# Kernel tuning notes

Measured on AMD Instinct MI355X. Metric: run time of the kernel, lower is better.

Reference implementation:

```python
import jax, jax.numpy as jnp
import numpy as np

D = 256      # hidden_dim / d_model
NH = 8       # num_heads
HD = D // NH # head_dim = 32
FF = 2048    # dim_feedforward
L = 2        # num_transformer_layers
CIN = 512
NC = 80      # num_classes
NA = 3       # num_anchors
EPS = 1e-5


def _ln(x, s, b):
    m = jnp.mean(x, axis=-1, keepdims=True)
    v = jnp.mean(jnp.square(x - m), axis=-1, keepdims=True)
    return (x - m) * jax.lax.rsqrt(v + EPS) * s + b


def setup_inputs() -> dict:
    key = jax.random.key(0)
    ks = iter(jax.random.split(key, 64))
    def g(shape, scale=0.02):
        return (jax.random.normal(next(ks), shape, dtype=jnp.float32) * scale)
    inp = {
        "x": jax.random.normal(next(ks), (4, CIN, 40, 40), dtype=jnp.float32),
        "conv_w": g((CIN, D)), "conv_b": jnp.zeros((D,), jnp.float32),
        "pos": jax.random.normal(next(ks), (1, D, 1, 1), dtype=jnp.float32),
        # stacked per-layer params [L, ...], weights stored as [in, out]
        "qw": g((L, D, D)), "qb": jnp.zeros((L, D)),
        "kw": g((L, D, D)), "kb": jnp.zeros((L, D)),
        "vw": g((L, D, D)), "vb": jnp.zeros((L, D)),
        "pw": g((L, D, D)), "pb": jnp.zeros((L, D)),
        "ln1s": jnp.ones((L, D)), "ln1b": jnp.zeros((L, D)),
        "ln2s": jnp.ones((L, D)), "ln2b": jnp.zeros((L, D)),
        "f1w": g((L, D, FF)), "f1b": jnp.zeros((L, FF)),
        "f2w": g((L, FF, D)), "f2b": jnp.zeros((L, D)),
        "cls_w1": g((D, D)), "cls_b1": jnp.zeros((D,)),
        "cls_w2": g((D, NA * NC)), "cls_b2": jnp.zeros((NA * NC,)),
        "box_w1": g((D, D)), "box_b1": jnp.zeros((D,)),
        "box_w2": g((D, NA * 4)), "box_b2": jnp.zeros((NA * 4,)),
        "obj_w1": g((D, D)), "obj_b1": jnp.zeros((D,)),
        "obj_w2": g((D, NA)), "obj_b2": jnp.zeros((NA,)),
    }
    return inp


def reference(x, conv_w, conv_b, pos, qw, qb, kw, kb, vw, vb, pw, pb,
              ln1s, ln1b, ln2s, ln2b, f1w, f1b, f2w, f2b,
              cls_w1, cls_b1, cls_w2, cls_b2,
              box_w1, box_b1, box_w2, box_b2,
              obj_w1, obj_b1, obj_w2, obj_b2):
    B, C, H, W = x.shape
    # 1x1 conv projection + positional encoding (broadcast scalar-per-channel)
    h = jnp.einsum('bchw,cd->bdhw', x, conv_w) + conv_b[None, :, None, None]
    h = h + pos  # broadcasts over B,H,W
    # flatten to sequence [B, N, D]
    N = H * W
    h = jnp.transpose(h.reshape(B, D, N), (0, 2, 1))

    scale = 1.0 / np.sqrt(HD)
    for i in range(L):
        # pre-norm MHSA
        y = _ln(h, ln1s[i], ln1b[i])
        q = (y @ qw[i] + qb[i]).reshape(B, N, NH, HD)
        k = (y @ kw[i] + kb[i]).reshape(B, N, NH, HD)
        v = (y @ vw[i] + vb[i]).reshape(B, N, NH, HD)
        scores = jnp.einsum('bnhd,bmhd->bhnm', q, k) * scale
        attn = jax.nn.softmax(scores, axis=-1)
        o = jnp.einsum('bhnm,bmhd->bnhd', attn, v).reshape(B, N, D)
        h = h + (o @ pw[i] + pb[i])
        # pre-norm FFN
        y = _ln(h, ln2s[i], ln2b[i])
        h = h + (jax.nn.relu(y @ f1w[i] + f1b[i]) @ f2w[i] + f2b[i])

    # prediction heads
    cls = jax.nn.relu(h @ cls_w1 + cls_b1) @ cls_w2 + cls_b2   # [B,N,NA*NC]
    box = jax.nn.relu(h @ box_w1 + box_b1) @ box_w2 + box_b2   # [B,N,NA*4]
    obj = jax.nn.relu(h @ obj_w1 + obj_b1) @ obj_w2 + obj_b2   # [B,N,NA]

    cls = jnp.transpose(cls.reshape(B, H, W, NA, NC), (0, 3, 1, 2, 4))
    box = jnp.transpose(box.reshape(B, H, W, NA, 4), (0, 3, 1, 2, 4))
    obj = jnp.transpose(obj.reshape(B, H, W, NA), (0, 3, 1, 2))
    return cls, box, obj
```

## Files before the change

### kernel.cpp

```cpp
#include <hip/hip_runtime.h>
#include <math.h>

#define BB   4
#define CIN  512
#define DD   256
#define NP   1600
#define TT   (BB*NP)
#define FF   2048
#define NHH  8
#define HDD  32
#define NA   3
#define NC   80

typedef __attribute__((ext_vector_type(8))) short bf16x8_t;
typedef __attribute__((ext_vector_type(4))) float f32x4_t;
typedef __attribute__((ext_vector_type(16))) float f32x16_t;

static __device__ __forceinline__ ushort f2bf(float f) {
    unsigned int u = __float_as_uint(f);
    u += 0x7FFF + ((u >> 16) & 1);
    return (ushort)(u >> 16);
}
static __device__ __forceinline__ float bf2f(ushort u) {
    return __uint_as_float((unsigned int)u << 16);
}
static __device__ __forceinline__ unsigned int cvt_pk_bf16(float lo, float hi) {
    unsigned int r;
    asm("v_cvt_pk_bf16_f32 %0, %1, %2" : "=v"(r) : "v"(lo), "v"(hi));
    return r;
}
static __device__ __forceinline__ void swap32(unsigned int& a, unsigned int& b) {
    asm("v_permlane32_swap_b32 %0, %1" : "+v"(a), "+v"(b));
}
static __device__ __forceinline__ bf16x8_t pack4(unsigned int a, unsigned int b,
                                                 unsigned int c, unsigned int d) {
    union { uint4 u; bf16x8_t v; } t;
    t.u = make_uint4(a, b, c, d);
    return t.v;
}

struct WDesc { const float* src; ushort* dst; int R; int C; int ntiles; float scale; };
struct WPrep { WDesc d[16]; };

__global__ __launch_bounds__(256) void wprep_kernel(WPrep p) {
    __shared__ float tile[32][33];
    int t = blockIdx.x;
    int i = 0;
    while (t >= p.d[i].ntiles) { t -= p.d[i].ntiles; i++; }
    const float* src = p.d[i].src;
    ushort* dst = p.d[i].dst;
    int R = p.d[i].R, C = p.d[i].C;
    float sc = p.d[i].scale;
    int tC = C >> 5;
    int r0 = (t / tC) * 32, c0 = (t % tC) * 32;
    int tx = threadIdx.x, ty = threadIdx.y;
    #pragma unroll
    for (int j = 0; j < 32; j += 8)
        tile[ty + j][tx] = src[(size_t)(r0 + ty + j) * C + (c0 + tx)];
    __syncthreads();
    #pragma unroll
    for (int j = 0; j < 32; j += 8)
        dst[(size_t)(c0 + ty + j) * R + (r0 + tx)] = f2bf(tile[tx][ty + j] * sc);
}

__global__ __launch_bounds__(256) void head2_wprep_kernel(
        const float* __restrict__ cls_w2, const float* __restrict__ box_w2,
        const float* __restrict__ obj_w2, ushort* __restrict__ dst)
{
    int nrow = blockIdx.x;
    int k = threadIdx.x;
    float v = 0.f;
    if (nrow < 240)                      v = cls_w2[k * 240 + nrow];
    else if (nrow >= 256 && nrow < 268)  v = box_w2[k * 12 + (nrow - 256)];
    else if (nrow >= 320 && nrow < 323)  v = obj_w2[k * 3 + (nrow - 320)];
    dst[(size_t)nrow * 256 + k] = f2bf(v);
}

__global__ void transpose_x_kernel(const float* __restrict__ x, ushort* __restrict__ xT) {
    __shared__ float tile[32][33];
    int b  = blockIdx.z;
    int c0 = blockIdx.x * 32;
    int n0 = blockIdx.y * 32;
    int tx = threadIdx.x, ty = threadIdx.y;
    #pragma unroll
    for (int j = 0; j < 32; j += 8) {
        tile[ty + j][tx] = x[b * CIN * NP + (c0 + ty + j) * NP + (n0 + tx)];
    }
    __syncthreads();
    #pragma unroll
    for (int j = 0; j < 32; j += 8) {
        xT[(size_t)(b * NP + n0 + ty + j) * CIN + (c0 + tx)] = f2bf(tile[tx][ty + j]);
    }
}

#define GEMM_CORE_LDA(A_, Bt_, K_, LDA_)                                         \
    __shared__ ushort As[64][72];                                                \
    __shared__ ushort Bs[64][72];                                                \
    int tid  = threadIdx.x;                                                      \
    int lane = tid & 63, wid = tid >> 6;                                         \
    int wm = wid >> 1, wn = wid & 1;                                             \
    int m0 = blockIdx.y * 64, n0 = blockIdx.x * 64;                              \
    int ln31 = lane & 31, lg = lane >> 5;                                        \
    int srow = tid >> 2;                                                         \
    int scol = (tid & 3) * 16;                                                   \
    const ushort* ag = (A_)  + (size_t)(m0 + srow) * (LDA_) + scol;              \
    const ushort* bg = (Bt_) + (size_t)(n0 + srow) * (K_) + scol;                \
    f32x16_t acc = {};                                                           \
    for (int k0 = 0; k0 < (K_); k0 += 64) {                                      \
        uint4 av0 = *(const uint4*)(ag + k0);                                    \
        uint4 av1 = *(const uint4*)(ag + k0 + 8);                                \
        uint4 bv0 = *(const uint4*)(bg + k0);                                    \
        uint4 bv1 = *(const uint4*)(bg + k0 + 8);                                \
        *(uint4*)&As[srow][scol]     = av0;                                      \
        *(uint4*)&As[srow][scol + 8] = av1;                                      \
        *(uint4*)&Bs[srow][scol]     = bv0;                                      \
        *(uint4*)&Bs[srow][scol + 8] = bv1;                                      \
        __syncthreads();                                                         \
        _Pragma("unroll")                                                        \
        for (int kc = 0; kc < 4; kc++) {                                         \
            bf16x8_t af = *(const bf16x8_t*)&As[wm * 32 + ln31][kc * 16 + lg * 8]; \
            bf16x8_t bf = *(const bf16x8_t*)&Bs[wn * 32 + ln31][kc * 16 + lg * 8]; \
            acc = __builtin_amdgcn_mfma_f32_32x32x16_bf16(af, bf, acc, 0, 0, 0); \
        }                                                                        \
        __syncthreads();                                                         \
    }                                                                            \
    int n = n0 + wn * 32 + ln31;

#define GEMM_CORE(A_, Bt_, K_) GEMM_CORE_LDA(A_, Bt_, K_, K_)

#define GEMM128_CORE(A_, Bt_, K_)                                                \
    __shared__ ushort As[128][72];                                               \
    __shared__ ushort Bs[128][72];                                               \
    int tid  = threadIdx.x;                                                      \
    int lane = tid & 63, wid = tid >> 6;                               \
    int wm = wid >> 2, wn = wid & 3;                                             \
    int m0 = blockIdx.y * 128, n0 = blockIdx.x * 128;                            \
    int ln31 = lane & 31, lg = lane >> 5;                                        \
    int srow = tid >> 2;                                             \
    int scol = (tid & 3) * 16;                                                   \
    const ushort* ag = (A_)  + (size_t)(m0 + srow) * (K_) + scol;                \
    const ushort* bg = (Bt_) + (size_t)(n0 + srow) * (K_) + scol;                \
    f32x16_t acc0 = {}, acc1 = {};                                               \
    for (int k0 = 0; k0 < (K_); k0 += 64) {                                      \
        uint4 av0 = *(const uint4*)(ag + k0);                                    \
        uint4 av1 = *(const uint4*)(ag + k0 + 8);                                \
        uint4 bv0 = *(const uint4*)(bg + k0);                                    \
        uint4 bv1 = *(const uint4*)(bg + k0 + 8);                                \
        *(uint4*)&As[srow][scol]     = av0;                                      \
        *(uint4*)&As[srow][scol + 8] = av1;                                      \
        *(uint4*)&Bs[srow][scol]     = bv0;                                      \
        *(uint4*)&Bs[srow][scol + 8] = bv1;                                      \
        __syncthreads();                                                         \
        _Pragma("unroll")                                                        \
        for (int kc = 0; kc < 4; kc++) {                                         \
            bf16x8_t af0 = *(const bf16x8_t*)&As[wm * 64 + ln31][kc * 16 + lg * 8];      \
            bf16x8_t af1 = *(const bf16x8_t*)&As[wm * 64 + 32 + ln31][kc * 16 + lg * 8]; \
            bf16x8_t bf  = *(const bf16x8_t*)&Bs[wn * 32 + ln31][kc * 16 + lg * 8];      \
            acc0 = __builtin_amdgcn_mfma_f32_32x32x16_bf16(af0, bf, acc0, 0, 0, 0);      \
            acc1 = __builtin_amdgcn_mfma_f32_32x32x16_bf16(af1, bf, acc1, 0, 0, 0);      \
        }                                                                        \
        __syncthreads();                                                         \
    }                                                                            \
    int n = n0 + wn * 32 + ln31;                                                 \
    int mbase = m0 + wm * 64;

__global__ __launch_bounds__(256) void gemm_mfma_kernel(
        const ushort* __restrict__ A, const ushort* __restrict__ Bt,
        const float* __restrict__ bias, const float* __restrict__ bias2,
        const float* __restrict__ residual, float* __restrict__ Cf,
        ushort* __restrict__ Cbf, int M, int N, int K, int do_relu)
{
    GEMM_CORE(A, Bt, K)
    float bsum = bias[n] + (bias2 ? bias2[n] : 0.f);
    #pragma unroll
    for (int r = 0; r < 16; r++) {
        int row = (r & 3) + 8 * (r >> 2) + 4 * lg;
        int m = m0 + wm * 32 + row;
        float v = acc[r] + bsum;
        if (do_relu) v = fmaxf(v, 0.f);
        if (residual) v += residual[(size_t)m * N + n];
        if (Cf)  Cf [(size_t)m * N + n] = v;
        if (Cbf) Cbf[(size_t)m * N + n] = f2bf(v);
    }
}

__global__ __launch_bounds__(512) void gemm128_qkv_kernel(
        const ushort* __restrict__ A, const ushort* __restrict__ Bt,
        const float* __restrict__ qb, const float* __restrict__ kb,
        const float* __restrict__ vb, ushort* __restrict__ q_out,
        ushort* __restrict__ k_out, ushort* __restrict__ vt_out, float qscale)
{
    GEMM128_CORE(A, Bt, DD)
    int seg = n >> 8;
    int c   = n & 255;
    if (seg == 0) {
        float bsum = qb[c] * qscale;
        #pragma unroll
        for (int r = 0; r < 16; r++) {
            int row = (r & 3) + 8 * (r >> 2) + 4 * lg;
            q_out[(size_t)(mbase + row) * DD + c]      = f2bf(acc0[r] + bsum);
            q_out[(size_t)(mbase + 32 + row) * DD + c] = f2bf(acc1[r] + bsum);
        }
    } else if (seg == 1) {
        float bsum = kb[c];
        #pragma unroll
        for (int r = 0; r < 16; r++) {
            int row = (r & 3) + 8 * (r >> 2) + 4 * lg;
            k_out[(size_t)(mbase + row) * DD + c]      = f2bf(acc0[r] + bsum);
            k_out[(size_t)(mbase + 32 + row) * DD + c] = f2bf(acc1[r] + bsum);
        }
    } else {
        float bsum = vb[c];
        int hh = c >> 5, d = c & 31;
        #pragma unroll
        for (int qq = 0; qq < 4; qq++) {
            int mq = mbase + 8 * qq + 4 * lg;
            int b0_ = mq / NP, nn0 = mq - b0_ * NP;
            ushort* vt0 = vt_out + ((size_t)(b0_ * NHH + hh) * HDD + d) * NP + nn0;
            *(ushort4*)vt0 = make_ushort4(
                f2bf(acc0[qq * 4 + 0] + bsum), f2bf(acc0[qq * 4 + 1] + bsum),
                f2bf(acc0[qq * 4 + 2] + bsum), f2bf(acc0[qq * 4 + 3] + bsum));
            int mq1 = mq + 32;
            int b1_ = mq1 / NP, nn1 = mq1 - b1_ * NP;
            ushort* vt1 = vt_out + ((size_t)(b1_ * NHH + hh) * HDD + d) * NP + nn1;
            *(ushort4*)vt1 = make_ushort4(
                f2bf(acc1[qq * 4 + 0] + bsum), f2bf(acc1[qq * 4 + 1] + bsum),
                f2bf(acc1[qq * 4 + 2] + bsum), f2bf(acc1[qq * 4 + 3] + bsum));
        }
    }
}

__global__ __launch_bounds__(512) void gemm128_ffn1_kernel(
        const ushort* __restrict__ A, const ushort* __restrict__ Bt,
        const float* __restrict__ bias, ushort* __restrict__ Cbf)
{
    GEMM128_CORE(A, Bt, DD)
    float bsum = bias[n];
    #pragma unroll
    for (int r = 0; r < 16; r++) {
        int row = (r & 3) + 8 * (r >> 2) + 4 * lg;
        Cbf[(size_t)(mbase + row) * FF + n]      = f2bf(fmaxf(acc0[r] + bsum, 0.f));
        Cbf[(size_t)(mbase + 32 + row) * FF + n] = f2bf(fmaxf(acc1[r] + bsum, 0.f));
    }
}

__global__ __launch_bounds__(512) void gemm128_head1_kernel(
        const ushort* __restrict__ A, const ushort* __restrict__ Bt,
        const float* __restrict__ b0, const float* __restrict__ b1,
        const float* __restrict__ b2, ushort* __restrict__ t1)
{
    GEMM128_CORE(A, Bt, DD)
    int seg = n >> 8;
    int c   = n & 255;
    float bsum = (seg == 0) ? b0[c] : (seg == 1) ? b1[c] : b2[c];
    #pragma unroll
    for (int r = 0; r < 16; r++) {
        int row = (r & 3) + 8 * (r >> 2) + 4 * lg;
        t1[(size_t)(mbase + row) * 768 + n]      = f2bf(fmaxf(acc0[r] + bsum, 0.f));
        t1[(size_t)(mbase + 32 + row) * 768 + n] = f2bf(fmaxf(acc1[r] + bsum, 0.f));
    }
}

__global__ __launch_bounds__(256) void gemm_head2_kernel(
        const ushort* __restrict__ t1, const ushort* __restrict__ Bt,
        const float* __restrict__ cb, const float* __restrict__ bb,
        const float* __restrict__ ob, float* __restrict__ cls_out,
        float* __restrict__ box_out, float* __restrict__ obj_out)
{
    int n0_ = blockIdx.x * 64;
    int seg_ = (n0_ >= 320) ? 2 : (n0_ >= 256) ? 1 : 0;
    const ushort* Aseg = t1 + seg_ * 256;
    GEMM_CORE_LDA(Aseg, Bt, 256, 768)

    float bsum = 0.f;
    float* outp = nullptr;
    int a_ = 0, s_ = 0, S_ = 1;
    if (seg_ == 0) {
        if (n < 240) { bsum = cb[n]; a_ = n / 80; s_ = n - a_ * 80; outp = cls_out; S_ = 80; }
    } else if (seg_ == 1) {
        int c = n - 256;
        if (c < 12) { bsum = bb[c]; a_ = c >> 2; s_ = c & 3; outp = box_out; S_ = 4; }
    } else {
        int c = n - 320;
        if (c < 3) { bsum = ob[c]; a_ = c; s_ = 0; outp = obj_out; S_ = 1; }
    }
    if (outp) {
        #pragma unroll
        for (int r = 0; r < 16; r++) {
            int row = (r & 3) + 8 * (r >> 2) + 4 * lg;
            int m = m0 + wm * 32 + row;
            int b = m / NP, hw = m - b * NP;
            outp[((size_t)(b * NA + a_) * NP + hw) * S_ + s_] = acc[r] + bsum;
        }
    }
}

__global__ __launch_bounds__(256) void ln_kernel(
        const float* __restrict__ x, const float* __restrict__ s,
        const float* __restrict__ b, ushort* __restrict__ y)
{
    int row = blockIdx.x;
    int t = threadIdx.x;
    float v = x[(size_t)row * DD + t];
    float s1 = v, s2 = v * v;
    #pragma unroll
    for (int m = 32; m >= 1; m >>= 1) {
        s1 += __shfl_xor(s1, m, 64);
        s2 += __shfl_xor(s2, m, 64);
    }
    __shared__ float w1[4], w2[4];
    int lane = t & 63, wid = t >> 6;
    if (lane == 0) { w1[wid] = s1; w2[wid] = s2; }
    __syncthreads();
    float S1 = w1[0] + w1[1] + w1[2] + w1[3];
    float S2 = w2[0] + w2[1] + w2[2] + w2[3];
    float mean = S1 * (1.f / DD);
    float var  = S2 * (1.f / DD) - mean * mean;
    float inv  = rsqrtf(var + 1e-5f);
    y[(size_t)row * DD + t] = f2bf((v - mean) * inv * s[t] + b[t]);
}

__global__ __launch_bounds__(320) void attn_mfma_kernel(
        const ushort* __restrict__ q, const ushort* __restrict__ k,
        const ushort* __restrict__ vt, ushort* __restrict__ o)
{
    __shared__ float mrg[5][64][36];
    int lane = threadIdx.x & 63;
    int wid  = threadIdx.x >> 6;
    int qq   = lane & 31;
    int hi   = lane >> 5;
    int h = blockIdx.y, b = blockIdx.z;
    int q0 = blockIdx.x * 64;
    int ks = wid * 320;

    const size_t tq = (size_t)(b * NP + q0 + qq) * DD + h * HDD;
    bf16x8_t qfA1 = *(const bf16x8_t*)(q + tq + hi * 8);
    bf16x8_t qfA2 = *(const bf16x8_t*)(q + tq + 16 + hi * 8);
    bf16x8_t qfB1 = *(const bf16x8_t*)(q + tq + (size_t)32 * DD + hi * 8);
    bf16x8_t qfB2 = *(const bf16x8_t*)(q + tq + (size_t)32 * DD + 16 + hi * 8);

    const ushort* kp = k + (size_t)(b * NP + qq) * DD + h * HDD + hi * 8;
    const ushort* vp = vt + ((size_t)(b * NHH + h) * HDD + qq) * NP + hi * 8;

    float lsumA = 0.f, lsumB = 0.f;
    f32x16_t otA = {};
    f32x16_t otB = {};

    bf16x8_t kf1 = *(const bf16x8_t*)(kp + (size_t)ks * DD);
    bf16x8_t kf2 = *(const bf16x8_t*)(kp + (size_t)ks * DD + 16);
    bf16x8_t vf1 = *(const bf16x8_t*)(vp + ks);
    bf16x8_t vf2 = *(const bf16x8_t*)(vp + ks + 16);

    for (int it = 0; it < 10; it++) {
        int kn = (it < 9) ? (ks + (it + 1) * 32) : ks;
        bf16x8_t nkf1 = *(const bf16x8_t*)(kp + (size_t)kn * DD);
        bf16x8_t nkf2 = *(const bf16x8_t*)(kp + (size_t)kn * DD + 16);
        bf16x8_t nvf1 = *(const bf16x8_t*)(vp + kn);
        bf16x8_t nvf2 = *(const bf16x8_t*)(vp + kn + 16);

        f32x16_t z = {};
        f32x16_t sA = __builtin_amdgcn_mfma_f32_32x32x16_bf16(kf1, qfA1, z, 0, 0, 0);
        sA = __builtin_amdgcn_mfma_f32_32x32x16_bf16(kf2, qfA2, sA, 0, 0, 0);
        f32x16_t sB = __builtin_amdgcn_mfma_f32_32x32x16_bf16(kf1, qfB1, z, 0, 0, 0);
        sB = __builtin_amdgcn_mfma_f32_32x32x16_bf16(kf2, qfB2, sB, 0, 0, 0);

        float pA[16], pB[16];
        #pragma unroll
        for (int r = 0; r < 16; r++) pA[r] = __builtin_amdgcn_exp2f(sA[r]);
        #pragma unroll
        for (int r = 0; r < 16; r++) pB[r] = __builtin_amdgcn_exp2f(sB[r]);
        lsumA += (((pA[0] + pA[1]) + (pA[2] + pA[3])) + ((pA[4] + pA[5]) + (pA[6] + pA[7])))
               + (((pA[8] + pA[9]) + (pA[10] + pA[11])) + ((pA[12] + pA[13]) + (pA[14] + pA[15])));
        lsumB += (((pB[0] + pB[1]) + (pB[2] + pB[3])) + ((pB[4] + pB[5]) + (pB[6] + pB[7])))
               + (((pB[8] + pB[9]) + (pB[10] + pB[11])) + ((pB[12] + pB[13]) + (pB[14] + pB[15])));

        unsigned int a0 = cvt_pk_bf16(pA[0],  pA[1]);
        unsigned int a1 = cvt_pk_bf16(pA[2],  pA[3]);
        unsigned int a2 = cvt_pk_bf16(pA[4],  pA[5]);
        unsigned int a3 = cvt_pk_bf16(pA[6],  pA[7]);
        unsigned int a4 = cvt_pk_bf16(pA[8],  pA[9]);
        unsigned int a5 = cvt_pk_bf16(pA[10], pA[11]);
        unsigned int a6 = cvt_pk_bf16(pA[12], pA[13]);
        unsigned int a7 = cvt_pk_bf16(pA[14], pA[15]);
        swap32(a2, a0); swap32(a3, a1); swap32(a6, a4); swap32(a7, a5);
        bf16x8_t pfA1 = pack4(a0, a1, a2, a3);
        bf16x8_t pfA2 = pack4(a4, a5, a6, a7);

        unsigned int b0 = cvt_pk_bf16(pB[0],  pB[1]);
        unsigned int b1 = cvt_pk_bf16(pB[2],  pB[3]);
        unsigned int b2 = cvt_pk_bf16(pB[4],  pB[5]);
        unsigned int b3 = cvt_pk_bf16(pB[6],  pB[7]);
        unsigned int b4 = cvt_pk_bf16(pB[8],  pB[9]);
        unsigned int b5 = cvt_pk_bf16(pB[10], pB[11]);
        unsigned int b6 = cvt_pk_bf16(pB[12], pB[13]);
        unsigned int b7 = cvt_pk_bf16(pB[14], pB[15]);
        swap32(b2, b0); swap32(b3, b1); swap32(b6, b4); swap32(b7, b5);
        bf16x8_t pfB1 = pack4(b0, b1, b2, b3);
        bf16x8_t pfB2 = pack4(b4, b5, b6, b7);

        otA = __builtin_amdgcn_mfma_f32_32x32x16_bf16(vf1, pfA1, otA, 0, 0, 0);
        otB = __builtin_amdgcn_mfma_f32_32x32x16_bf16(vf1, pfB1, otB, 0, 0, 0);
        otA = __builtin_amdgcn_mfma_f32_32x32x16_bf16(vf2, pfA2, otA, 0, 0, 0);
        otB = __builtin_amdgcn_mfma_f32_32x32x16_bf16(vf2, pfB2, otB, 0, 0, 0);

        kf1 = nkf1; kf2 = nkf2; vf1 = nvf1; vf2 = nvf2;
    }

    lsumA += __shfl_xor(lsumA, 32, 64);
    lsumB += __shfl_xor(lsumB, 32, 64);

    #pragma unroll
    for (int r = 0; r < 16; r++) mrg[wid][lane][r] = otA[r];
    mrg[wid][lane][16] = lsumA;
    #pragma unroll
    for (int r = 0; r < 16; r++) mrg[wid][lane][18 + r] = otB[r];
    mrg[wid][lane][34] = lsumB;
    __syncthreads();

    if (wid < 2) {
        int off = wid * 18;
        float ov[16] = {};
        float L = 0.f;
        #pragma unroll
        for (int w = 0; w < 5; w++) {
            #pragma unroll
            for (int r = 0; r < 16; r++) ov[r] += mrg[w][lane][off + r];
            L += mrg[w][lane][off + 16];
        }
        float inv = 1.f / L;
        size_t tqo = tq + (size_t)wid * 32 * DD;
        #pragma unroll
        for (int i = 0; i < 4; i++) {
            ushort4 s4 = make_ushort4(f2bf(ov[4 * i + 0] * inv), f2bf(ov[4 * i + 1] * inv),
                                      f2bf(ov[4 * i + 2] * inv), f2bf(ov[4 * i + 3] * inv));
            *(ushort4*)(o + tqo + 8 * i + 4 * hi) = s4;
        }
    }
}

static inline void launch_gemm(const ushort* A, const ushort* Bt, const float* bias,
                               const float* bias2, const float* res, float* Cf,
                               ushort* Cbf, int M, int N, int K, int relu,
                               hipStream_t s) {
    dim3 g(N / 64, M / 64), b(256);
    hipLaunchKernelGGL(gemm_mfma_kernel, g, b, 0, s,
                       A, Bt, bias, bias2, res, Cf, Cbf, M, N, K, relu);
}

extern "C" void kernel_launch(void* const* d_in, const int* in_sizes, int n_in,
                              void* d_out, int out_size, void* d_ws, size_t ws_size,
                              hipStream_t stream) {
    const float* x      = (const float*)d_in[0];
    const float* conv_w = (const float*)d_in[1];
    const float* conv_b = (const float*)d_in[2];
    const float* pos    = (const float*)d_in[3];
    const float* qw     = (const float*)d_in[4];
    const float* qb     = (const float*)d_in[5];
    const float* kw     = (const float*)d_in[6];
    const float* kb     = (const float*)d_in[7];
    const float* vw     = (const float*)d_in[8];
    const float* vb     = (const float*)d_in[9];
    const float* pw     = (const float*)d_in[10];
    const float* pb     = (const float*)d_in[11];
    const float* ln1s   = (const float*)d_in[12];
    const float* ln1b   = (const float*)d_in[13];
    const float* ln2s   = (const float*)d_in[14];
    const float* ln2b   = (const float*)d_in[15];
    const float* f1w    = (const float*)d_in[16];
    const float* f1b    = (const float*)d_in[17];
    const float* f2w    = (const float*)d_in[18];
    const float* f2b    = (const float*)d_in[19];
    const float* cls_w1 = (const float*)d_in[20];
    const float* cls_b1 = (const float*)d_in[21];
    const float* cls_w2 = (const float*)d_in[22];
    const float* cls_b2 = (const float*)d_in[23];
    const float* box_w1 = (const float*)d_in[24];
    const float* box_b1 = (const float*)d_in[25];
    const float* box_w2 = (const float*)d_in[26];
    const float* box_b2 = (const float*)d_in[27];
    const float* obj_w1 = (const float*)d_in[28];
    const float* obj_b1 = (const float*)d_in[29];
    const float* obj_w2 = (const float*)d_in[30];
    const float* obj_b2 = (const float*)d_in[31];

    float* out = (float*)d_out;
    const size_t TD = (size_t)TT * DD;

    char* p = (char*)d_ws;
    auto alloc = [&](size_t bytes) { char* r = p; p += (bytes + 255) & ~(size_t)255; return r; };
    float*  h    = (float*) alloc(TD * 4);
    ushort* y    = (ushort*)alloc(TD * 2);
    ushort* qB   = (ushort*)alloc(TD * 2);
    ushort* kB   = (ushort*)alloc(TD * 2);
    ushort* Vt   = (ushort*)alloc(TD * 2);
    ushort* oB   = (ushort*)alloc(TD * 2);
    ushort* hbf  = (ushort*)alloc(TD * 2);
    ushort* ffn  = (ushort*)alloc((size_t)TT * FF * 2);
    ushort* xT   = (ushort*)alloc((size_t)TT * CIN * 2);
    ushort* wT   = (ushort*)alloc((size_t)(2949120 + 98304) * 2);
    ushort* t1   = ffn;

    ushort* convT  = wT;
    ushort* qkvT   = wT + 131072;
    ushort* pwT    = wT + 524288;
    ushort* f1wT   = wT + 655360;
    ushort* f2wT   = wT + 1703936;
    ushort* headT  = wT + 2752512;
    ushort* head2T = wT + 2949120;

    const float QSCALE = 0.17677669529663687f * 1.4426950408889634f;

    WPrep wp;
    int total_tiles = 0;
    auto setd = [&](int i, const float* src, ushort* dst, int R, int C, float sc) {
        wp.d[i] = {src, dst, R, C, (R / 32) * (C / 32), sc};
        total_tiles += wp.d[i].ntiles;
    };
    setd(0,  conv_w, convT, CIN, DD, 1.f);
    setd(1,  qw,            qkvT,                    DD, DD, QSCALE);
    setd(2,  kw,            qkvT + 65536,            DD, DD, 1.f);
    setd(3,  vw,            qkvT + 131072,           DD, DD, 1.f);
    setd(4,  qw + DD * DD,  qkvT + 196608,           DD, DD, QSCALE);
    setd(5,  kw + DD * DD,  qkvT + 196608 + 65536,   DD, DD, 1.f);
    setd(6,  vw + DD * DD,  qkvT + 196608 + 131072,  DD, DD, 1.f);
    setd(7,  pw,            pwT,            DD, DD, 1.f);
    setd(8,  pw + DD * DD,  pwT + DD * DD,  DD, DD, 1.f);
    setd(9,  f1w,           f1wT,           DD, FF, 1.f);
    setd(10, f1w + DD * FF, f1wT + DD * FF, DD, FF, 1.f);
    setd(11, f2w,           f2wT,           FF, DD, 1.f);
    setd(12, f2w + FF * DD, f2wT + FF * DD, FF, DD, 1.f);
    setd(13, cls_w1, headT,          DD, DD, 1.f);
    setd(14, box_w1, headT + 65536,  DD, DD, 1.f);
    setd(15, obj_w1, headT + 131072, DD, DD, 1.f);
    hipLaunchKernelGGL(wprep_kernel, dim3(total_tiles), dim3(32, 8), 0, stream, wp);
    hipLaunchKernelGGL(head2_wprep_kernel, dim3(384), dim3(256), 0, stream,
                       cls_w2, box_w2, obj_w2, head2T);

    hipLaunchKernelGGL(transpose_x_kernel, dim3(CIN / 32, NP / 32, BB), dim3(32, 8),
                       0, stream, x, xT);

    launch_gemm(xT, convT, conv_b, pos, nullptr, h, nullptr, TT, DD, CIN, 0, stream);

    for (int i = 0; i < 2; i++) {
        hipLaunchKernelGGL(ln_kernel, dim3(TT), dim3(DD), 0, stream,
                           h, ln1s + i * DD, ln1b + i * DD, y);
        hipLaunchKernelGGL(gemm128_qkv_kernel, dim3(768 / 128, TT / 128), dim3(512), 0, stream,
                           y, qkvT + (size_t)i * 196608, qb + i * DD, kb + i * DD,
                           vb + i * DD, qB, kB, Vt, QSCALE);

        hipLaunchKernelGGL(attn_mfma_kernel, dim3(NP / 64, NHH, BB), dim3(320), 0, stream,
                           qB, kB, Vt, oB);

        launch_gemm(oB, pwT + (size_t)i * DD * DD, pb + i * DD, nullptr, h, h, nullptr,
                    TT, DD, DD, 0, stream);

        hipLaunchKernelGGL(ln_kernel, dim3(TT), dim3(DD), 0, stream,
                           h, ln2s + i * DD, ln2b + i * DD, y);
        hipLaunchKernelGGL(gemm128_ffn1_kernel, dim3(FF / 128, TT / 128), dim3(512), 0, stream,
                           y, f1wT + (size_t)i * DD * FF, f1b + i * FF, ffn);

        launch_gemm(ffn, f2wT + (size_t)i * FF * DD, f2b + i * DD, nullptr, h,
                    (i == 0) ? h : nullptr, (i == 1) ? hbf : nullptr,
                    TT, DD, FF, 0, stream);
    }

    hipLaunchKernelGGL(gemm128_head1_kernel, dim3(768 / 128, TT / 128), dim3(512), 0, stream,
                       hbf, headT, cls_b1, box_b1, obj_b1, t1);

    float* cls_out = out;
    float* box_out = out + (size_t)BB * NA * NP * NC;
    float* obj_out = box_out + (size_t)BB * NA * NP * 4;

    hipLaunchKernelGGL(gemm_head2_kernel, dim3(384 / 64, TT / 64), dim3(256), 0, stream,
                       t1, head2T, cls_b2, box_b2, obj_b2, cls_out, box_out, obj_out);
}
```

Measured before the change: 257.5 us.

## Widen attention query tile to five 32-row tiles per block to reuse K/V loads

Each attention block now handles 160 queries (five 32-row MFMA tiles) instead of 64, so every K/V fragment loaded per wave feeds five score/PV tile computations. This cuts K/V global traffic per query, and the grid shrinks to 10x8x4 = 320 blocks. The merge across the five key-split waves now runs in five rounds with a smaller shared buffer and extra barriers. The cost is higher register pressure from five accumulators and reduced block-level parallelism.

```diff
diff --git a/kernel.cpp b/kernel.cpp
--- a/kernel.cpp
+++ b/kernel.cpp
@@ -324,27 +324,29 @@
         const ushort* __restrict__ q, const ushort* __restrict__ k,
         const ushort* __restrict__ vt, ushort* __restrict__ o)
 {
-    __shared__ float mrg[5][64][36];
+    __shared__ float mrg[5][64][18];
     int lane = threadIdx.x & 63;
     int wid  = threadIdx.x >> 6;
     int qq   = lane & 31;
     int hi   = lane >> 5;
     int h = blockIdx.y, b = blockIdx.z;
-    int q0 = blockIdx.x * 64;
+    int q0 = blockIdx.x * 160;
     int ks = wid * 320;
 
-    const size_t tq = (size_t)(b * NP + q0 + qq) * DD + h * HDD;
-    bf16x8_t qfA1 = *(const bf16x8_t*)(q + tq + hi * 8);
-    bf16x8_t qfA2 = *(const bf16x8_t*)(q + tq + 16 + hi * 8);
-    bf16x8_t qfB1 = *(const bf16x8_t*)(q + tq + (size_t)32 * DD + hi * 8);
-    bf16x8_t qfB2 = *(const bf16x8_t*)(q + tq + (size_t)32 * DD + 16 + hi * 8);
+    const size_t tqbase = (size_t)(b * NP + q0 + qq) * DD + h * HDD;
+
+    bf16x8_t qf1[5], qf2[5];
+    #pragma unroll
+    for (int t = 0; t < 5; t++) {
+        qf1[t] = *(const bf16x8_t*)(q + tqbase + (size_t)(32 * t) * DD + hi * 8);
+        qf2[t] = *(const bf16x8_t*)(q + tqbase + (size_t)(32 * t) * DD + 16 + hi * 8);
+    }
 
     const ushort* kp = k + (size_t)(b * NP + qq) * DD + h * HDD + hi * 8;
     const ushort* vp = vt + ((size_t)(b * NHH + h) * HDD + qq) * NP + hi * 8;
 
-    float lsumA = 0.f, lsumB = 0.f;
-    f32x16_t otA = {};
-    f32x16_t otB = {};
+    float lsum[5] = {0.f, 0.f, 0.f, 0.f, 0.f};
+    f32x16_t ot0 = {}, ot1 = {}, ot2 = {}, ot3 = {}, ot4 = {};
 
     bf16x8_t kf1 = *(const bf16x8_t*)(kp + (size_t)ks * DD);
     bf16x8_t kf2 = *(const bf16x8_t*)(kp + (size_t)ks * DD + 16);
@@ -358,84 +360,76 @@
         bf16x8_t nvf1 = *(const bf16x8_t*)(vp + kn);
         bf16x8_t nvf2 = *(const bf16x8_t*)(vp + kn + 16);
 
-        f32x16_t z = {};
-        f32x16_t sA = __builtin_amdgcn_mfma_f32_32x32x16_bf16(kf1, qfA1, z, 0, 0, 0);
-        sA = __builtin_amdgcn_mfma_f32_32x32x16_bf16(kf2, qfA2, sA, 0, 0, 0);
-        f32x16_t sB = __builtin_amdgcn_mfma_f32_32x32x16_bf16(kf1, qfB1, z, 0, 0, 0);
-        sB = __builtin_amdgcn_mfma_f32_32x32x16_bf16(kf2, qfB2, sB, 0, 0, 0);
-
-        float pA[16], pB[16];
-        #pragma unroll
-        for (int r = 0; r < 16; r++) pA[r] = __builtin_amdgcn_exp2f(sA[r]);
-        #pragma unroll
-        for (int r = 0; r < 16; r++) pB[r] = __builtin_amdgcn_exp2f(sB[r]);
-        lsumA += (((pA[0] + pA[1]) + (pA[2] + pA[3])) + ((pA[4] + pA[5]) + (pA[6] + pA[7])))
-               + (((pA[8] + pA[9]) + (pA[10] + pA[11])) + ((pA[12] + pA[13]) + (pA[14] + pA[15])));
-        lsumB += (((pB[0] + pB[1]) + (pB[2] + pB[3])) + ((pB[4] + pB[5]) + (pB[6] + pB[7])))
-               + (((pB[8] + pB[9]) + (pB[10] + pB[11])) + ((pB[12] + pB[13]) + (pB[14] + pB[15])));
-
-        unsigned int a0 = cvt_pk_bf16(pA[0],  pA[1]);
-        unsigned int a1 = cvt_pk_bf16(pA[2],  pA[3]);
-        unsigned int a2 = cvt_pk_bf16(pA[4],  pA[5]);
-        unsigned int a3 = cvt_pk_bf16(pA[6],  pA[7]);
-        unsigned int a4 = cvt_pk_bf16(pA[8],  pA[9]);
-        unsigned int a5 = cvt_pk_bf16(pA[10], pA[11]);
-        unsigned int a6 = cvt_pk_bf16(pA[12], pA[13]);
-        unsigned int a7 = cvt_pk_bf16(pA[14], pA[15]);
-        swap32(a2, a0); swap32(a3, a1); swap32(a6, a4); swap32(a7, a5);
-        bf16x8_t pfA1 = pack4(a0, a1, a2, a3);
-        bf16x8_t pfA2 = pack4(a4, a5, a6, a7);
-
-        unsigned int b0 = cvt_pk_bf16(pB[0],  pB[1]);
-        unsigned int b1 = cvt_pk_bf16(pB[2],  pB[3]);
-        unsigned int b2 = cvt_pk_bf16(pB[4],  pB[5]);
-        unsigned int b3 = cvt_pk_bf16(pB[6],  pB[7]);
-        unsigned int b4 = cvt_pk_bf16(pB[8],  pB[9]);
-        unsigned int b5 = cvt_pk_bf16(pB[10], pB[11]);
-        unsigned int b6 = cvt_pk_bf16(pB[12], pB[13]);
-        unsigned int b7 = cvt_pk_bf16(pB[14], pB[15]);
-        swap32(b2, b0); swap32(b3, b1); swap32(b6, b4); swap32(b7, b5);
-        bf16x8_t pfB1 = pack4(b0, b1, b2, b3);
-        bf16x8_t pfB2 = pack4(b4, b5, b6, b7);
-
-        otA = __builtin_amdgcn_mfma_f32_32x32x16_bf16(vf1, pfA1, otA, 0, 0, 0);
-        otB = __builtin_amdgcn_mfma_f32_32x32x16_bf16(vf1, pfB1, otB, 0, 0, 0);
-        otA = __builtin_amdgcn_mfma_f32_32x32x16_bf16(vf2, pfA2, otA, 0, 0, 0);
-        otB = __builtin_amdgcn_mfma_f32_32x32x16_bf16(vf2, pfB2, otB, 0, 0, 0);
+#define ATTN_TILE(T, OT)                                                        \
+        {                                                                       \
+            f32x16_t z = {};                                                    \
+            f32x16_t s = __builtin_amdgcn_mfma_f32_32x32x16_bf16(kf1, qf1[T], z, 0, 0, 0); \
+            s = __builtin_amdgcn_mfma_f32_32x32x16_bf16(kf2, qf2[T], s, 0, 0, 0);          \
+            float p[16];                                                        \
+            _Pragma("unroll")                                                   \
+            for (int r = 0; r < 16; r++) p[r] = __builtin_amdgcn_exp2f(s[r]);   \
+            lsum[T] += (((p[0] + p[1]) + (p[2] + p[3])) + ((p[4] + p[5]) + (p[6] + p[7])))   \
+                     + (((p[8] + p[9]) + (p[10] + p[11])) + ((p[12] + p[13]) + (p[14] + p[15]))); \
+            unsigned int w0 = cvt_pk_bf16(p[0],  p[1]);                         \
+            unsigned int w1 = cvt_pk_bf16(p[2],  p[3]);                         \
+            unsigned int w2 = cvt_pk_bf16(p[4],  p[5]);                         \
+            unsigned int w3 = cvt_pk_bf16(p[6],  p[7]);                         \
+            unsigned int w4 = cvt_pk_bf16(p[8],  p[9]);                         \
+            unsigned int w5 = cvt_pk_bf16(p[10], p[11]);                        \
+            unsigned int w6 = cvt_pk_bf16(p[12], p[13]);                        \
+            unsigned int w7 = cvt_pk_bf16(p[14], p[15]);                        \
+            swap32(w2, w0); swap32(w3, w1); swap32(w6, w4); swap32(w7, w5);     \
+            bf16x8_t pf1 = pack4(w0, w1, w2, w3);                               \
+            bf16x8_t pf2 = pack4(w4, w5, w6, w7);                               \
+            OT = __builtin_amdgcn_mfma_f32_32x32x16_bf16(vf1, pf1, OT, 0, 0, 0);\
+            OT = __builtin_amdgcn_mfma_f32_32x32x16_bf16(vf2, pf2, OT, 0, 0, 0);\
+        }
+        ATTN_TILE(0, ot0)
+        ATTN_TILE(1, ot1)
+        ATTN_TILE(2, ot2)
+        ATTN_TILE(3, ot3)
+        ATTN_TILE(4, ot4)
+#undef ATTN_TILE
 
         kf1 = nkf1; kf2 = nkf2; vf1 = nvf1; vf2 = nvf2;
     }
 
-    lsumA += __shfl_xor(lsumA, 32, 64);
-    lsumB += __shfl_xor(lsumB, 32, 64);
-
-    #pragma unroll
-    for (int r = 0; r < 16; r++) mrg[wid][lane][r] = otA[r];
-    mrg[wid][lane][16] = lsumA;
-    #pragma unroll
-    for (int r = 0; r < 16; r++) mrg[wid][lane][18 + r] = otB[r];
-    mrg[wid][lane][34] = lsumB;
-    __syncthreads();
-
-    if (wid < 2) {
-        int off = wid * 18;
-        float ov[16] = {};
-        float L = 0.f;
-        #pragma unroll
-        for (int w = 0; w < 5; w++) {
-            #pragma unroll
-            for (int r = 0; r < 16; r++) ov[r] += mrg[w][lane][off + r];
-            L += mrg[w][lane][off + 16];
-        }
-        float inv = 1.f / L;
-        size_t tqo = tq + (size_t)wid * 32 * DD;
-        #pragma unroll
-        for (int i = 0; i < 4; i++) {
-            ushort4 s4 = make_ushort4(f2bf(ov[4 * i + 0] * inv), f2bf(ov[4 * i + 1] * inv),
-                                      f2bf(ov[4 * i + 2] * inv), f2bf(ov[4 * i + 3] * inv));
-            *(ushort4*)(o + tqo + 8 * i + 4 * hi) = s4;
-        }
-    }
+    #pragma unroll
+    for (int t = 0; t < 5; t++) lsum[t] += __shfl_xor(lsum[t], 32, 64);
+
+#define MERGE_ROUND(T, OT)                                                      \
+    {                                                                           \
+        _Pragma("unroll")                                                       \
+        for (int r = 0; r < 16; r++) mrg[wid][lane][r] = OT[r];                 \
+        mrg[wid][lane][16] = lsum[T];                                           \
+        __syncthreads();                                                        \
+        if (wid == T) {                                                         \
+            float ov[16] = {};                                                  \
+            float L = 0.f;                                                      \
+            _Pragma("unroll")                                                   \
+            for (int w = 0; w < 5; w++) {                                       \
+                _Pragma("unroll")                                               \
+                for (int r = 0; r < 16; r++) ov[r] += mrg[w][lane][r];          \
+                L += mrg[w][lane][16];                                          \
+            }                                                                   \
+            float inv = 1.f / L;                                                \
+            size_t tqo = tqbase + (size_t)(32 * T) * DD;                        \
+            _Pragma("unroll")                                                   \
+            for (int i = 0; i < 4; i++) {                                       \
+                ushort4 s4 = make_ushort4(                                      \
+                    f2bf(ov[4 * i + 0] * inv), f2bf(ov[4 * i + 1] * inv),       \
+                    f2bf(ov[4 * i + 2] * inv), f2bf(ov[4 * i + 3] * inv));      \
+                *(ushort4*)(o + tqo + 8 * i + 4 * hi) = s4;                     \
+            }                                                                   \
+        }                                                                       \
+        __syncthreads();                                                        \
+    }
+    MERGE_ROUND(0, ot0)
+    MERGE_ROUND(1, ot1)
+    MERGE_ROUND(2, ot2)
+    MERGE_ROUND(3, ot3)
+    MERGE_ROUND(4, ot4)
+#undef MERGE_ROUND
 }
 
 static inline void launch_gemm(const ushort* A, const ushort* Bt, const float* bias,
@@ -548,7 +542,7 @@
                            y, qkvT + (size_t)i * 196608, qb + i * DD, kb + i * DD,
                            vb + i * DD, qB, kB, Vt, QSCALE);
 
-        hipLaunchKernelGGL(attn_mfma_kernel, dim3(NP / 64, NHH, BB), dim3(320), 0, stream,
+        hipLaunchKernelGGL(attn_mfma_kernel, dim3(NP / 160, NHH, BB), dim3(320), 0, stream,
                            qB, kB, Vt, oB);
 
         launch_gemm(oB, pwT + (size_t)i * DD * DD, pb + i * DD, nullptr, h, h, nullptr,
```

Result: slower. 293.4 us (+14.0%).
